# Kernel optimization log

Hardware: AMD Instinct MI355X
Metric: run time of the kernel (lower is better)

The kernel has to match this reference:

```python
import jax, jax.numpy as jnp
import numpy as np

EPS = 1e-5  # torch LayerNorm default eps

def _mish(x):
    return x * jnp.tanh(jax.nn.softplus(x))

def _ln(x, g, b):
    mu = jnp.mean(x, axis=-1, keepdims=True)
    var = jnp.mean(jnp.square(x - mu), axis=-1, keepdims=True)
    return (x - mu) * jax.lax.rsqrt(var + EPS) * g + b

def setup_inputs() -> dict:
    key = jax.random.key(0)
    ks = jax.random.split(key, 10)
    B, D, O1, O2, O3 = 65536, 784, 512, 264, 128
    def lin(k, fan_in, shape):
        bound = 1.0 / np.sqrt(fan_in)
        return jax.random.uniform(k, shape, jnp.float32, -bound, bound)
    return {
        "x":  jax.random.uniform(ks[0], (B, D), jnp.float32),
        "W1": lin(ks[1], D,  (O1, D)),   # enFC1, bias=False
        "g1": jnp.ones((O1,), jnp.float32), "b1": jnp.zeros((O1,), jnp.float32),
        "W2": lin(ks[2], O1, (O2, O1)),  # enFC2, bias=False
        "g2": jnp.ones((O2,), jnp.float32), "b2": jnp.zeros((O2,), jnp.float32),
        "W3": lin(ks[3], O2, (O3, O2)),  # enFC3 with bias
        "b3": lin(ks[4], O2, (O3,)),
        "gh": jnp.ones((O3,), jnp.float32), "bh": jnp.zeros((O3,), jnp.float32),
        "D1": lin(ks[5], O3, (O2, O3)),  # deFC1, bias=False
        "g3": jnp.ones((O2,), jnp.float32), "b3n": jnp.zeros((O2,), jnp.float32),
        "D2": lin(ks[6], O2, (O1, O2)),  # deFC2, bias=False
        "g4": jnp.ones((O1,), jnp.float32), "b4": jnp.zeros((O1,), jnp.float32),
        "D3": lin(ks[7], O1, (D, O1)),   # deFC3 with bias
        "bo": lin(ks[8], O1, (D,)),
    }

def reference(x, W1, g1, b1, W2, g2, b2, W3, b3, gh, bh,
              D1, g3, b3n, D2, g4, b4, D3, bo):
    h = _mish(_ln(x @ W1.T, g1, b1))
    h = _mish(_ln(h @ W2.T, g2, b2))
    x_latent = _mish(_ln(h @ W3.T + b3, gh, bh))
    h = _mish(_ln(x_latent @ D1.T, g3, b3n))
    h = _mish(_ln(h @ D2.T, g4, b4))
    out = jax.nn.sigmoid(h @ D3.T + bo)
    return out, jnp.sum(jnp.abs(x_latent))
```

## Files before the change

kernel.cpp:

```cpp
#include <hip/hip_runtime.h>


typedef short bf16x8 __attribute__((ext_vector_type(8)));
typedef float f32x4  __attribute__((ext_vector_type(4)));

#define B_ROWS 65536
#define EPS_LN 1e-5f

static __device__ __forceinline__ unsigned short f2bf(float f) {
    union { float f; unsigned u; } v; v.f = f;
    unsigned r = v.u + 0x7FFFu + ((v.u >> 16) & 1u);
    return (unsigned short)(r >> 16);
}

static __device__ __forceinline__ float mish_f(float x) {
    if (x > 15.f) return x;
    float u = __expf(x);
    float p = __fmaf_rn(u, u, 2.f * u);
    return x * (p / (p + 2.f));
}

static __device__ __forceinline__ void glds16(const void* g, void* l) {
    typedef __attribute__((address_space(3))) unsigned lds_u32;
    typedef __attribute__((address_space(1))) const unsigned glb_u32;
    lds_u32* lp = (lds_u32*)l;
    unsigned lofs = __builtin_amdgcn_readfirstlane((unsigned)(unsigned long long)lp);
    lp = (lds_u32*)(unsigned long long)lofs;
    __builtin_amdgcn_global_load_lds((glb_u32*)g, lp, 16, 0, 0);
}

struct CvtArgs {
    const float* src[6];
    unsigned short* dst[6];
    int O[6], K[6], KP[6];
    int base[7];
};

__global__ void wpad_kernel(CvtArgs a) {
    int b = blockIdx.x;
    int seg = 0;
    while (b >= a.base[seg + 1]) ++seg;
    int r = b - a.base[seg];
    int O = a.O[seg], K = a.K[seg], KP = a.KP[seg];
    const float* s = a.src[seg];
    unsigned short* d = a.dst[seg];
    for (int c = threadIdx.x; c < KP; c += 256) {
        unsigned short v = 0;
        if (r < O && c < K) v = f2bf(s[(size_t)r * K + c]);
        d[(size_t)r * KP + c] = v;
    }
}

template<int KP, int ASTR, int BN, int OREAL, int OSTRIDE, int NKT,
         bool SRCF32, bool HASBIAS, bool ABS, bool LN>
__global__ __launch_bounds__(512, 2)
void layer9(const void* __restrict__ Asrc,
            const unsigned short* __restrict__ Wp,
            const float* __restrict__ gam,
            const float* __restrict__ bet,
            const float* __restrict__ bias,
            void* __restrict__ Aout,
            float* __restrict__ partials)
{
    constexpr int NT   = BN / 64;
    constexpr int NCHW = BN / 8;
    constexpr int NCH  = NCHW + (SRCF32 ? 0 : 16);
    constexpr int MAXC = (NCH + 7) / 8;
    constexpr int ABY  = 128 * 128;
    constexpr int WBY  = BN * 128;

    __shared__ __align__(16) char smem[2 * ABY + 2 * WBY];

    const int tid  = threadIdx.x;
    const int lane = tid & 63;
    const int wu   = __builtin_amdgcn_readfirstlane(tid >> 6);
    const int wr = wu >> 2, wc = wu & 3;
    const int lg = lane >> 4, lc = lane & 15;
    const int row0  = blockIdx.x * 128;
    const int cbase = LN ? 0 : blockIdx.y * BN;

    const int crow = lane >> 3;
    const int sg   = (lane & 7) ^ crow;
    const size_t vofW = ((size_t)crow * KP + (size_t)(sg << 3)) * 2;
    const size_t vofA = ((size_t)crow * ASTR + (size_t)(sg << 3)) * 2;

    auto stage = [&](int t, int b) {
#pragma unroll
        for (int i = 0; i < MAXC; ++i) {
            int c = wu + 8 * i;
            if (c < NCHW) {
                const char* g = (const char*)Wp +
                    ((size_t)(cbase + c * 8) * KP) * 2 + (size_t)t * 128 + vofW;
                glds16(g, smem + (2 * ABY + b * WBY + c * 1024));
            } else if (c < NCH) {
                int ca = c - NCHW;
                const char* g = (const char*)Asrc +
                    ((size_t)(row0 + ca * 8) * ASTR) * 2 + (size_t)t * 128 + vofA;
                glds16(g, smem + (b * ABY + ca * 1024));
            }
        }
    };

    const int ar = tid >> 2, as = tid & 3;
    const float* axp = (const float*)Asrc + (size_t)(row0 + ar) * ASTR + as * 16;
    float4 rA[4];
#pragma unroll
    for (int j = 0; j < 4; ++j) rA[j] = make_float4(0, 0, 0, 0);

    auto loadA1 = [&](int t) {
#pragma unroll
        for (int j = 0; j < 4; ++j) {
            int c0 = t * 64 + as * 16 + j * 4;
            rA[j] = (c0 + 3 < 784) ? *(const float4*)(axp + t * 64 + j * 4)
                                   : make_float4(0, 0, 0, 0);
        }
    };
    auto pubA = [&](int b) {
        union { unsigned short us[8]; uint4 v; } u0, u1;
        u0.us[0] = f2bf(rA[0].x); u0.us[1] = f2bf(rA[0].y);
        u0.us[2] = f2bf(rA[0].z); u0.us[3] = f2bf(rA[0].w);
        u0.us[4] = f2bf(rA[1].x); u0.us[5] = f2bf(rA[1].y);
        u0.us[6] = f2bf(rA[1].z); u0.us[7] = f2bf(rA[1].w);
        u1.us[0] = f2bf(rA[2].x); u1.us[1] = f2bf(rA[2].y);
        u1.us[2] = f2bf(rA[2].z); u1.us[3] = f2bf(rA[2].w);
        u1.us[4] = f2bf(rA[3].x); u1.us[5] = f2bf(rA[3].y);
        u1.us[6] = f2bf(rA[3].z); u1.us[7] = f2bf(rA[3].w);
        int s0 = as * 2, rb = b * ABY + ar * 128, rx = ar & 7;
        *(uint4*)(smem + rb + (((s0    ) ^ rx) << 4)) = u0.v;
        *(uint4*)(smem + rb + (((s0 + 1) ^ rx) << 4)) = u1.v;
    };

    stage(0, 0);
    if constexpr (SRCF32) { loadA1(0); pubA(0); }
    __syncthreads();

    f32x4 acc[4][NT];
#pragma unroll
    for (int a = 0; a < 4; ++a)
#pragma unroll
        for (int c = 0; c < NT; ++c) acc[a][c] = (f32x4){0.f, 0.f, 0.f, 0.f};

    const int f0 = ((lg ^ (lc & 7)) << 4);

    for (int t = 0; t < NKT; ++t) {
        const int bsel = t & 1;
        if (t + 1 < NKT) {
            stage(t + 1, bsel ^ 1);
            if constexpr (SRCF32) loadA1(t + 1);
        }
        const char* Ab = smem + bsel * ABY + (wr * 64 + lc) * 128;
        const char* Bb = smem + 2 * ABY + bsel * WBY + (wc * NT * 16 + lc) * 128;
#pragma unroll
        for (int h = 0; h < 2; ++h) {
            const int fh = f0 ^ (h << 6);
            bf16x8 afr[4], bfr[NT];
#pragma unroll
            for (int a = 0; a < 4; ++a)
                afr[a] = *(const bf16x8*)(Ab + a * 2048 + fh);
#pragma unroll
            for (int c = 0; c < NT; ++c)
                bfr[c] = *(const bf16x8*)(Bb + c * 2048 + fh);
            __builtin_amdgcn_s_setprio(1);
#pragma unroll
            for (int c = 0; c < NT; ++c)
#pragma unroll
                for (int a = 0; a < 4; ++a)
                    acc[a][c] = __builtin_amdgcn_mfma_f32_16x16x32_bf16(afr[a], bfr[c], acc[a][c], 0, 0, 0);
            __builtin_amdgcn_s_setprio(0);
        }
        if constexpr (SRCF32) { if (t + 1 < NKT) pubA(bsel ^ 1); }
        __syncthreads();
    }

    if constexpr (LN) {
        if constexpr (HASBIAS) {
#pragma unroll
            for (int c = 0; c < NT; ++c) {
                int col = wc * NT * 16 + c * 16 + lc;
                float bv = (col < OREAL) ? bias[col] : 0.f;
#pragma unroll
                for (int a = 0; a < 4; ++a)
#pragma unroll
                    for (int r = 0; r < 4; ++r) acc[a][c][r] += bv;
            }
        }
        float ps1[4][4], ps2[4][4];
#pragma unroll
        for (int a = 0; a < 4; ++a)
#pragma unroll
            for (int r = 0; r < 4; ++r) { ps1[a][r] = 0.f; ps2[a][r] = 0.f; }
#pragma unroll
        for (int a = 0; a < 4; ++a)
#pragma unroll
            for (int c = 0; c < NT; ++c)
#pragma unroll
                for (int r = 0; r < 4; ++r) {
                    float v = acc[a][c][r];
                    ps1[a][r] += v;
                    ps2[a][r] = __fmaf_rn(v, v, ps2[a][r]);
                }
#pragma unroll
        for (int m = 1; m < 16; m <<= 1)
#pragma unroll
            for (int a = 0; a < 4; ++a)
#pragma unroll
                for (int r = 0; r < 4; ++r) {
                    ps1[a][r] += __shfl_xor(ps1[a][r], m);
                    ps2[a][r] += __shfl_xor(ps2[a][r], m);
                }

        float* lnP  = (float*)smem;
        float* lnMR = (float*)(smem + 4096);
        float* wsum = (float*)(smem + 5120);

        if (lc == 0) {
#pragma unroll
            for (int a = 0; a < 4; ++a)
#pragma unroll
                for (int r = 0; r < 4; ++r) {
                    int row = wr * 64 + a * 16 + lg * 4 + r;
                    lnP[row * 4 + wc]       = ps1[a][r];
                    lnP[512 + row * 4 + wc] = ps2[a][r];
                }
        }
        __syncthreads();
        if (tid < 128) {
            float s1 = lnP[tid * 4] + lnP[tid * 4 + 1] + lnP[tid * 4 + 2] + lnP[tid * 4 + 3];
            float s2 = lnP[512 + tid * 4] + lnP[512 + tid * 4 + 1] +
                       lnP[512 + tid * 4 + 2] + lnP[512 + tid * 4 + 3];
            float mu = s1 * (1.f / OREAL);
            float var = fmaxf(s2 * (1.f / OREAL) - mu * mu, 0.f);
            lnMR[tid]       = mu;
            lnMR[128 + tid] = rsqrtf(var + EPS_LN);
        }
        __syncthreads();

        float gcol[NT], bcol[NT];
#pragma unroll
        for (int c = 0; c < NT; ++c) {
            int col = wc * NT * 16 + c * 16 + lc;
            gcol[c] = (col < OREAL) ? gam[col] : 0.f;
            bcol[c] = (col < OREAL) ? bet[col] : 0.f;
        }

        float asum = 0.f;
        unsigned short* outp = (unsigned short*)Aout;
#pragma unroll
        for (int a = 0; a < 4; ++a)
#pragma unroll
            for (int r = 0; r < 4; ++r) {
                int rl = wr * 64 + a * 16 + lg * 4 + r;
                float mu = lnMR[rl], rs = lnMR[128 + rl];
                size_t rowoff = (size_t)(row0 + rl) * OSTRIDE;
#pragma unroll
                for (int c = 0; c < NT; ++c) {
                    int col = wc * NT * 16 + c * 16 + lc;
                    if (col < OSTRIDE) {
                        unsigned short outv = 0;
                        if (col < OREAL) {
                            float v = (acc[a][c][r] - mu) * rs * gcol[c] + bcol[c];
                            float mz = mish_f(v);
                            if (ABS) asum += fabsf(mz);
                            outv = f2bf(mz);
                        }
                        outp[rowoff + col] = outv;
                    }
                }
            }

        if constexpr (ABS) {
#pragma unroll
            for (int m = 1; m < 64; m <<= 1) asum += __shfl_xor(asum, m);
            if (lane == 0) wsum[wu] = asum;
            __syncthreads();
            if (tid == 0) {
                float s = 0.f;
                for (int w = 0; w < 8; ++w) s += wsum[w];
                partials[blockIdx.x] = s;
            }
        }
    } else {
        float* outp = (float*)Aout;
#pragma unroll
        for (int c = 0; c < NT; ++c) {
            int col = cbase + wc * NT * 16 + c * 16 + lc;
            bool ok = col < OREAL;
            float bv = ok ? bias[col] : 0.f;
#pragma unroll
            for (int a = 0; a < 4; ++a)
#pragma unroll
                for (int r = 0; r < 4; ++r) {
                    if (ok) {
                        int rl = wr * 64 + a * 16 + lg * 4 + r;
                        float v = acc[a][c][r] + bv;
                        outp[(size_t)(row0 + rl) * OSTRIDE + col] = 1.f / (1.f + __expf(-v));
                    }
                }
        }
    }
}

__global__ void reduce_abs(const float* __restrict__ partials, float* __restrict__ out) {
    __shared__ float sm[256];
    float s = 0.f;
    for (int i = threadIdx.x; i < 512; i += 256) s += partials[i];
    sm[threadIdx.x] = s;
    __syncthreads();
    for (int step = 128; step > 0; step >>= 1) {
        if (threadIdx.x < step) sm[threadIdx.x] += sm[threadIdx.x + step];
        __syncthreads();
    }
    if (threadIdx.x == 0) out[0] = sm[0];
}

extern "C" void kernel_launch(void* const* d_in, const int* in_sizes, int n_in,
                              void* d_out, int out_size, void* d_ws, size_t ws_size,
                              hipStream_t stream)
{
    const float* x   = (const float*)d_in[0];
    const float* W1  = (const float*)d_in[1];
    const float* g1  = (const float*)d_in[2];
    const float* b1  = (const float*)d_in[3];
    const float* W2  = (const float*)d_in[4];
    const float* g2  = (const float*)d_in[5];
    const float* b2  = (const float*)d_in[6];
    const float* W3  = (const float*)d_in[7];
    const float* b3  = (const float*)d_in[8];
    const float* gh  = (const float*)d_in[9];
    const float* bh  = (const float*)d_in[10];
    const float* D1  = (const float*)d_in[11];
    const float* g3  = (const float*)d_in[12];
    const float* b3n = (const float*)d_in[13];
    const float* D2  = (const float*)d_in[14];
    const float* g4  = (const float*)d_in[15];
    const float* b4  = (const float*)d_in[16];
    const float* D3  = (const float*)d_in[17];
    const float* bo  = (const float*)d_in[18];

    char* ws = (char*)d_ws;
    size_t off = 0;
    auto alloc = [&](size_t bytes) -> char* {
        char* p = ws + off;
        off += (bytes + 255) & ~(size_t)255;
        return p;
    };
    unsigned short* W1p = (unsigned short*)alloc((size_t)512 * 832 * 2);
    unsigned short* W2p = (unsigned short*)alloc((size_t)384 * 512 * 2);
    unsigned short* W3p = (unsigned short*)alloc((size_t)128 * 320 * 2);
    unsigned short* D1p = (unsigned short*)alloc((size_t)384 * 128 * 2);
    unsigned short* D2p = (unsigned short*)alloc((size_t)512 * 320 * 2);
    unsigned short* D3p = (unsigned short*)alloc((size_t)896 * 512 * 2);
    unsigned short* actP = (unsigned short*)alloc((size_t)B_ROWS * 512 * 2);
    unsigned short* actQ = (unsigned short*)alloc((size_t)B_ROWS * 320 * 2);
    unsigned short* actL = (unsigned short*)alloc((size_t)B_ROWS * 128 * 2);
    float* partials = (float*)alloc(512 * 4);

    CvtArgs ca;
    ca.src[0] = W1; ca.dst[0] = W1p; ca.O[0] = 512; ca.K[0] = 784; ca.KP[0] = 832;
    ca.src[1] = W2; ca.dst[1] = W2p; ca.O[1] = 264; ca.K[1] = 512; ca.KP[1] = 512;
    ca.src[2] = W3; ca.dst[2] = W3p; ca.O[2] = 128; ca.K[2] = 264; ca.KP[2] = 320;
    ca.src[3] = D1; ca.dst[3] = D1p; ca.O[3] = 264; ca.K[3] = 128; ca.KP[3] = 128;
    ca.src[4] = D2; ca.dst[4] = D2p; ca.O[4] = 512; ca.K[4] = 264; ca.KP[4] = 320;
    ca.src[5] = D3; ca.dst[5] = D3p; ca.O[5] = 784; ca.K[5] = 512; ca.KP[5] = 512;
    ca.base[0] = 0;    ca.base[1] = 512;  ca.base[2] = 896;
    ca.base[3] = 1024; ca.base[4] = 1408; ca.base[5] = 1920; ca.base[6] = 2816;
    wpad_kernel<<<2816, 256, 0, stream>>>(ca);

    const int NB = B_ROWS / 128;

    layer9<832, 784, 512, 512, 512, 13, true,  false, false, true>
        <<<NB, 512, 0, stream>>>(x, W1p, g1, b1, nullptr, actP, nullptr);
    layer9<512, 512, 384, 264, 320, 8,  false, false, false, true>
        <<<NB, 512, 0, stream>>>(actP, W2p, g2, b2, nullptr, actQ, nullptr);
    layer9<320, 320, 128, 128, 128, 5,  false, true,  true,  true>
        <<<NB, 512, 0, stream>>>(actQ, W3p, gh, bh, b3, actL, partials);
    layer9<128, 128, 384, 264, 320, 2,  false, false, false, true>
        <<<NB, 512, 0, stream>>>(actL, D1p, g3, b3n, nullptr, actQ, nullptr);
    layer9<320, 320, 512, 512, 512, 5,  false, false, false, true>
        <<<NB, 512, 0, stream>>>(actQ, D2p, g4, b4, nullptr, actP, nullptr);
    dim3 g6(NB, 2);
    layer9<512, 512, 448, 784, 784, 8,  false, true,  false, false>
        <<<g6, 512, 0, stream>>>(actP, D3p, nullptr, nullptr, bo, d_out, nullptr);

    reduce_abs<<<1, 256, 0, stream>>>(partials, (float*)d_out + (size_t)B_ROWS * 784);
}
```

Measured before the change: 426.9 us.

## Split K-loop into four barriered phases interleaving staging with MFMA

Restructures the GEMM main loop of every layer into four sub-phases (two K-halves times two column halves). Global-to-LDS staging is split into two groups issued between phases, with explicit s_barrier and lgkmcnt/vmcnt waits replacing the single __syncthreads. The fp32 input load for the first layer is prefetched two tiles ahead. The aim is to overlap memory traffic with matrix-core work and keep the waves in step, at the cost of more barriers and tighter hand-written wait counts, which could break correctness or stall if the counts are wrong.

```diff
diff --git a/kernel.cpp b/kernel.cpp
--- a/kernel.cpp
+++ b/kernel.cpp
@@ -28,6 +28,16 @@
     lp = (lds_u32*)(unsigned long long)lofs;
     __builtin_amdgcn_global_load_lds((glb_u32*)g, lp, 16, 0, 0);
 }
+
+template<int N> __device__ __forceinline__ void vwait() {
+    if constexpr      (N <= 0) asm volatile("s_waitcnt vmcnt(0)" ::: "memory");
+    else if constexpr (N == 4) asm volatile("s_waitcnt vmcnt(4)" ::: "memory");
+    else                       asm volatile("s_waitcnt vmcnt(8)" ::: "memory");
+}
+
+#define LGKM0 do { asm volatile("s_waitcnt lgkmcnt(0)" ::: "memory"); \
+                   __builtin_amdgcn_sched_barrier(0); } while (0)
+#define PBAR  __builtin_amdgcn_s_barrier()
 
 struct CvtArgs {
     const float* src[6];
@@ -54,18 +64,19 @@
 template<int KP, int ASTR, int BN, int OREAL, int OSTRIDE, int NKT,
          bool SRCF32, bool HASBIAS, bool ABS, bool LN>
 __global__ __launch_bounds__(512, 2)
-void layer9(const void* __restrict__ Asrc,
-            const unsigned short* __restrict__ Wp,
-            const float* __restrict__ gam,
-            const float* __restrict__ bet,
-            const float* __restrict__ bias,
-            void* __restrict__ Aout,
-            float* __restrict__ partials)
+void layer10(const void* __restrict__ Asrc,
+             const unsigned short* __restrict__ Wp,
+             const float* __restrict__ gam,
+             const float* __restrict__ bet,
+             const float* __restrict__ bias,
+             void* __restrict__ Aout,
+             float* __restrict__ partials)
 {
     constexpr int NT   = BN / 64;
+    constexpr int CH0  = (NT + 1) / 2;
+    constexpr int CH1  = NT - CH0;
     constexpr int NCHW = BN / 8;
-    constexpr int NCH  = NCHW + (SRCF32 ? 0 : 16);
-    constexpr int MAXC = (NCH + 7) / 8;
+    constexpr int NWCH = NCHW / 8;
     constexpr int ABY  = 128 * 128;
     constexpr int WBY  = BN * 128;
 
@@ -84,20 +95,21 @@
     const size_t vofW = ((size_t)crow * KP + (size_t)(sg << 3)) * 2;
     const size_t vofA = ((size_t)crow * ASTR + (size_t)(sg << 3)) * 2;
 
-    auto stage = [&](int t, int b) {
-#pragma unroll
-        for (int i = 0; i < MAXC; ++i) {
-            int c = wu + 8 * i;
-            if (c < NCHW) {
-                const char* g = (const char*)Wp +
+    auto stage_grp = [&](int t, int b, int g) {
+#pragma unroll
+        for (int i = 0; i < NWCH; ++i) {
+            if ((i & 1) == g) {
+                int c = wu + 8 * i;
+                const char* gp = (const char*)Wp +
                     ((size_t)(cbase + c * 8) * KP) * 2 + (size_t)t * 128 + vofW;
-                glds16(g, smem + (2 * ABY + b * WBY + c * 1024));
-            } else if (c < NCH) {
-                int ca = c - NCHW;
-                const char* g = (const char*)Asrc +
-                    ((size_t)(row0 + ca * 8) * ASTR) * 2 + (size_t)t * 128 + vofA;
-                glds16(g, smem + (b * ABY + ca * 1024));
+                glds16(gp, smem + (2 * ABY + b * WBY + c * 1024));
             }
+        }
+        if constexpr (!SRCF32) {
+            int ca = wu + 8 * g;
+            const char* gp = (const char*)Asrc +
+                ((size_t)(row0 + ca * 8) * ASTR) * 2 + (size_t)t * 128 + vofA;
+            glds16(gp, smem + (b * ABY + ca * 1024));
         }
     };
 
@@ -130,8 +142,12 @@
         *(uint4*)(smem + rb + (((s0 + 1) ^ rx) << 4)) = u1.v;
     };
 
-    stage(0, 0);
-    if constexpr (SRCF32) { loadA1(0); pubA(0); }
+    stage_grp(0, 0, 0);
+    stage_grp(0, 0, 1);
+    if constexpr (SRCF32) {
+        loadA1(0); pubA(0);
+        if (NKT > 1) loadA1(1);
+    }
     __syncthreads();
 
     f32x4 acc[4][NT];
@@ -143,33 +159,71 @@
     const int f0 = ((lg ^ (lc & 7)) << 4);
 
     for (int t = 0; t < NKT; ++t) {
-        const int bsel = t & 1;
-        if (t + 1 < NKT) {
-            stage(t + 1, bsel ^ 1);
-            if constexpr (SRCF32) loadA1(t + 1);
-        }
+        const int bsel = t & 1, nb = bsel ^ 1;
+        const bool pre = (t + 1 < NKT);
         const char* Ab = smem + bsel * ABY + (wr * 64 + lc) * 128;
         const char* Bb = smem + 2 * ABY + bsel * WBY + (wc * NT * 16 + lc) * 128;
-#pragma unroll
-        for (int h = 0; h < 2; ++h) {
-            const int fh = f0 ^ (h << 6);
-            bf16x8 afr[4], bfr[NT];
-#pragma unroll
-            for (int a = 0; a < 4; ++a)
-                afr[a] = *(const bf16x8*)(Ab + a * 2048 + fh);
-#pragma unroll
-            for (int c = 0; c < NT; ++c)
-                bfr[c] = *(const bf16x8*)(Bb + c * 2048 + fh);
-            __builtin_amdgcn_s_setprio(1);
-#pragma unroll
-            for (int c = 0; c < NT; ++c)
-#pragma unroll
-                for (int a = 0; a < 4; ++a)
-                    acc[a][c] = __builtin_amdgcn_mfma_f32_16x16x32_bf16(afr[a], bfr[c], acc[a][c], 0, 0, 0);
-            __builtin_amdgcn_s_setprio(0);
-        }
-        if constexpr (SRCF32) { if (t + 1 < NKT) pubA(bsel ^ 1); }
-        __syncthreads();
+
+        bf16x8 afr[4], bfr0[CH0], bfr1[CH1 > 0 ? CH1 : 1];
+
+#pragma unroll
+        for (int a = 0; a < 4; ++a) afr[a] = *(const bf16x8*)(Ab + a * 2048 + f0);
+#pragma unroll
+        for (int c = 0; c < CH0; ++c) bfr0[c] = *(const bf16x8*)(Bb + c * 2048 + f0);
+        if (pre) stage_grp(t + 1, nb, 0);
+        PBAR; LGKM0;
+        __builtin_amdgcn_s_setprio(1);
+#pragma unroll
+        for (int c = 0; c < CH0; ++c)
+#pragma unroll
+            for (int a = 0; a < 4; ++a)
+                acc[a][c] = __builtin_amdgcn_mfma_f32_16x16x32_bf16(afr[a], bfr0[c], acc[a][c], 0, 0, 0);
+        __builtin_amdgcn_s_setprio(0);
+        PBAR;
+
+#pragma unroll
+        for (int c = 0; c < CH1; ++c) bfr1[c] = *(const bf16x8*)(Bb + (CH0 + c) * 2048 + f0);
+        if (pre) stage_grp(t + 1, nb, 1);
+        PBAR; LGKM0;
+        __builtin_amdgcn_s_setprio(1);
+#pragma unroll
+        for (int c = 0; c < CH1; ++c)
+#pragma unroll
+            for (int a = 0; a < 4; ++a)
+                acc[a][CH0 + c] = __builtin_amdgcn_mfma_f32_16x16x32_bf16(afr[a], bfr1[c], acc[a][CH0 + c], 0, 0, 0);
+        __builtin_amdgcn_s_setprio(0);
+        PBAR;
+
+#pragma unroll
+        for (int a = 0; a < 4; ++a) afr[a] = *(const bf16x8*)(Ab + a * 2048 + (f0 ^ 64));
+#pragma unroll
+        for (int c = 0; c < CH0; ++c) bfr0[c] = *(const bf16x8*)(Bb + c * 2048 + (f0 ^ 64));
+        PBAR; LGKM0;
+        __builtin_amdgcn_s_setprio(1);
+#pragma unroll
+        for (int c = 0; c < CH0; ++c)
+#pragma unroll
+            for (int a = 0; a < 4; ++a)
+                acc[a][c] = __builtin_amdgcn_mfma_f32_16x16x32_bf16(afr[a], bfr0[c], acc[a][c], 0, 0, 0);
+        __builtin_amdgcn_s_setprio(0);
+        PBAR;
+
+#pragma unroll
+        for (int c = 0; c < CH1; ++c) bfr1[c] = *(const bf16x8*)(Bb + (CH0 + c) * 2048 + (f0 ^ 64));
+        if constexpr (SRCF32) {
+            if (pre) pubA(nb);
+            if (t + 2 < NKT) loadA1(t + 2);
+        }
+        PBAR; LGKM0;
+        __builtin_amdgcn_s_setprio(1);
+#pragma unroll
+        for (int c = 0; c < CH1; ++c)
+#pragma unroll
+            for (int a = 0; a < 4; ++a)
+                acc[a][CH0 + c] = __builtin_amdgcn_mfma_f32_16x16x32_bf16(afr[a], bfr1[c], acc[a][CH0 + c], 0, 0, 0);
+        __builtin_amdgcn_s_setprio(0);
+        vwait<SRCF32 ? 4 : 0>();
+        PBAR;
     }
 
     if constexpr (LN) {
@@ -368,18 +422,18 @@
 
     const int NB = B_ROWS / 128;
 
-    layer9<832, 784, 512, 512, 512, 13, true,  false, false, true>
+    layer10<832, 784, 512, 512, 512, 13, true,  false, false, true>
         <<<NB, 512, 0, stream>>>(x, W1p, g1, b1, nullptr, actP, nullptr);
-    layer9<512, 512, 384, 264, 320, 8,  false, false, false, true>
+    layer10<512, 512, 384, 264, 320, 8,  false, false, false, true>
         <<<NB, 512, 0, stream>>>(actP, W2p, g2, b2, nullptr, actQ, nullptr);
-    layer9<320, 320, 128, 128, 128, 5,  false, true,  true,  true>
+    layer10<320, 320, 128, 128, 128, 5,  false, true,  true,  true>
         <<<NB, 512, 0, stream>>>(actQ, W3p, gh, bh, b3, actL, partials);
-    layer9<128, 128, 384, 264, 320, 2,  false, false, false, true>
+    layer10<128, 128, 384, 264, 320, 2,  false, false, false, true>
         <<<NB, 512, 0, stream>>>(actL, D1p, g3, b3n, nullptr, actQ, nullptr);
-    layer9<320, 320, 512, 512, 512, 5,  false, false, false, true>
+    layer10<320, 320, 512, 512, 512, 5,  false, false, false, true>
         <<<NB, 512, 0, stream>>>(actQ, D2p, g4, b4, nullptr, actP, nullptr);
     dim3 g6(NB, 2);
-    layer9<512, 512, 448, 784, 784, 8,  false, true,  false, false>
+    layer10<512, 512, 448, 784, 784, 8,  false, true,  false, false>
         <<<g6, 512, 0, stream>>>(actP, D3p, nullptr, nullptr, bo, d_out, nullptr);
 
     reduce_abs<<<1, 256, 0, stream>>>(partials, (float*)d_out + (size_t)B_ROWS * 784);
```

New measurement: 431.8 us. About the same (+1.1%).

## Switch GEMM tiles to 32x32x16 MFMA and split final layer launch

Applied to the files above, without the earlier changes.

Each wave now computes its output tile with 32x32x16 bf16 MFMA blocks (2 row blocks × BN/128 column blocks) instead of 16x16x32 blocks. The LDS fragment loads, swizzle offsets, LayerNorm row reductions and epilogue row and column mapping are all rewritten for the 32x32 accumulator layout. The larger MFMA shape cuts LDS fragment reads and instruction count per flop, and the wider shuffle reduction covers 32 lanes. The last decoder layer also changes from one 2-D grid with 448-column halves to two launches of 512 and 384 columns with an explicit column base, which adds a kernel launch.

```diff
diff --git a/kernel.cpp b/kernel.cpp
--- a/kernel.cpp
+++ b/kernel.cpp
@@ -1,8 +1,8 @@
 #include <hip/hip_runtime.h>
 
 
-typedef short bf16x8 __attribute__((ext_vector_type(8)));
-typedef float f32x4  __attribute__((ext_vector_type(4)));
+typedef short bf16x8  __attribute__((ext_vector_type(8)));
+typedef float f32x16  __attribute__((ext_vector_type(16)));
 
 #define B_ROWS 65536
 #define EPS_LN 1e-5f
@@ -54,15 +54,16 @@
 template<int KP, int ASTR, int BN, int OREAL, int OSTRIDE, int NKT,
          bool SRCF32, bool HASBIAS, bool ABS, bool LN>
 __global__ __launch_bounds__(512, 2)
-void layer9(const void* __restrict__ Asrc,
-            const unsigned short* __restrict__ Wp,
-            const float* __restrict__ gam,
-            const float* __restrict__ bet,
-            const float* __restrict__ bias,
-            void* __restrict__ Aout,
-            float* __restrict__ partials)
+void layer11(const void* __restrict__ Asrc,
+             const unsigned short* __restrict__ Wp,
+             const float* __restrict__ gam,
+             const float* __restrict__ bet,
+             const float* __restrict__ bias,
+             void* __restrict__ Aout,
+             float* __restrict__ partials,
+             int cbase)
 {
-    constexpr int NT   = BN / 64;
+    constexpr int CI   = BN / 128;
     constexpr int NCHW = BN / 8;
     constexpr int NCH  = NCHW + (SRCF32 ? 0 : 16);
     constexpr int MAXC = (NCH + 7) / 8;
@@ -75,9 +76,8 @@
     const int lane = tid & 63;
     const int wu   = __builtin_amdgcn_readfirstlane(tid >> 6);
     const int wr = wu >> 2, wc = wu & 3;
-    const int lg = lane >> 4, lc = lane & 15;
-    const int row0  = blockIdx.x * 128;
-    const int cbase = LN ? 0 : blockIdx.y * BN;
+    const int l31 = lane & 31, h = lane >> 5;
+    const int row0 = blockIdx.x * 128;
 
     const int crow = lane >> 3;
     const int sg   = (lane & 7) ^ crow;
@@ -134,13 +134,17 @@
     if constexpr (SRCF32) { loadA1(0); pubA(0); }
     __syncthreads();
 
-    f32x4 acc[4][NT];
-#pragma unroll
-    for (int a = 0; a < 4; ++a)
-#pragma unroll
-        for (int c = 0; c < NT; ++c) acc[a][c] = (f32x4){0.f, 0.f, 0.f, 0.f};
-
-    const int f0 = ((lg ^ (lc & 7)) << 4);
+    f32x16 acc[2][CI];
+#pragma unroll
+    for (int ri = 0; ri < 2; ++ri)
+#pragma unroll
+        for (int ci = 0; ci < CI; ++ci)
+#pragma unroll
+            for (int e = 0; e < 16; ++e) acc[ri][ci][e] = 0.f;
+
+    int swz[4];
+#pragma unroll
+    for (int ks = 0; ks < 4; ++ks) swz[ks] = (((ks * 2 + h) ^ (l31 & 7)) << 4);
 
     for (int t = 0; t < NKT; ++t) {
         const int bsel = t & 1;
@@ -148,24 +152,24 @@
             stage(t + 1, bsel ^ 1);
             if constexpr (SRCF32) loadA1(t + 1);
         }
-        const char* Ab = smem + bsel * ABY + (wr * 64 + lc) * 128;
-        const char* Bb = smem + 2 * ABY + bsel * WBY + (wc * NT * 16 + lc) * 128;
-#pragma unroll
-        for (int h = 0; h < 2; ++h) {
-            const int fh = f0 ^ (h << 6);
-            bf16x8 afr[4], bfr[NT];
-#pragma unroll
-            for (int a = 0; a < 4; ++a)
-                afr[a] = *(const bf16x8*)(Ab + a * 2048 + fh);
-#pragma unroll
-            for (int c = 0; c < NT; ++c)
-                bfr[c] = *(const bf16x8*)(Bb + c * 2048 + fh);
+        const char* Ab = smem + bsel * ABY + (wr * 64 + l31) * 128;
+        const char* Bb = smem + 2 * ABY + bsel * WBY + (wc * CI * 32 + l31) * 128;
+#pragma unroll
+        for (int ks = 0; ks < 4; ++ks) {
+            bf16x8 afr[2], bfr[CI];
+#pragma unroll
+            for (int ri = 0; ri < 2; ++ri)
+                afr[ri] = *(const bf16x8*)(Ab + ri * 4096 + swz[ks]);
+#pragma unroll
+            for (int ci = 0; ci < CI; ++ci)
+                bfr[ci] = *(const bf16x8*)(Bb + ci * 4096 + swz[ks]);
             __builtin_amdgcn_s_setprio(1);
 #pragma unroll
-            for (int c = 0; c < NT; ++c)
-#pragma unroll
-                for (int a = 0; a < 4; ++a)
-                    acc[a][c] = __builtin_amdgcn_mfma_f32_16x16x32_bf16(afr[a], bfr[c], acc[a][c], 0, 0, 0);
+            for (int ci = 0; ci < CI; ++ci)
+#pragma unroll
+                for (int ri = 0; ri < 2; ++ri)
+                    acc[ri][ci] = __builtin_amdgcn_mfma_f32_32x32x16_bf16(
+                        afr[ri], bfr[ci], acc[ri][ci], 0, 0, 0);
             __builtin_amdgcn_s_setprio(0);
         }
         if constexpr (SRCF32) { if (t + 1 < NKT) pubA(bsel ^ 1); }
@@ -175,53 +179,48 @@
     if constexpr (LN) {
         if constexpr (HASBIAS) {
 #pragma unroll
-            for (int c = 0; c < NT; ++c) {
-                int col = wc * NT * 16 + c * 16 + lc;
+            for (int ci = 0; ci < CI; ++ci) {
+                int col = wc * CI * 32 + ci * 32 + l31;
                 float bv = (col < OREAL) ? bias[col] : 0.f;
 #pragma unroll
-                for (int a = 0; a < 4; ++a)
-#pragma unroll
-                    for (int r = 0; r < 4; ++r) acc[a][c][r] += bv;
-            }
-        }
-        float ps1[4][4], ps2[4][4];
-#pragma unroll
-        for (int a = 0; a < 4; ++a)
-#pragma unroll
-            for (int r = 0; r < 4; ++r) { ps1[a][r] = 0.f; ps2[a][r] = 0.f; }
-#pragma unroll
-        for (int a = 0; a < 4; ++a)
-#pragma unroll
-            for (int c = 0; c < NT; ++c)
-#pragma unroll
-                for (int r = 0; r < 4; ++r) {
-                    float v = acc[a][c][r];
-                    ps1[a][r] += v;
-                    ps2[a][r] = __fmaf_rn(v, v, ps2[a][r]);
-                }
-#pragma unroll
-        for (int m = 1; m < 16; m <<= 1)
-#pragma unroll
-            for (int a = 0; a < 4; ++a)
-#pragma unroll
-                for (int r = 0; r < 4; ++r) {
-                    ps1[a][r] += __shfl_xor(ps1[a][r], m);
-                    ps2[a][r] += __shfl_xor(ps2[a][r], m);
-                }
+                for (int ri = 0; ri < 2; ++ri)
+#pragma unroll
+                    for (int r = 0; r < 16; ++r) acc[ri][ci][r] += bv;
+            }
+        }
 
         float* lnP  = (float*)smem;
         float* lnMR = (float*)(smem + 4096);
         float* wsum = (float*)(smem + 5120);
 
-        if (lc == 0) {
-#pragma unroll
-            for (int a = 0; a < 4; ++a)
-#pragma unroll
-                for (int r = 0; r < 4; ++r) {
-                    int row = wr * 64 + a * 16 + lg * 4 + r;
-                    lnP[row * 4 + wc]       = ps1[a][r];
-                    lnP[512 + row * 4 + wc] = ps2[a][r];
-                }
+#pragma unroll
+        for (int ri = 0; ri < 2; ++ri) {
+            float s1[16], s2[16];
+#pragma unroll
+            for (int r = 0; r < 16; ++r) { s1[r] = 0.f; s2[r] = 0.f; }
+#pragma unroll
+            for (int ci = 0; ci < CI; ++ci)
+#pragma unroll
+                for (int r = 0; r < 16; ++r) {
+                    float v = acc[ri][ci][r];
+                    s1[r] += v;
+                    s2[r] = __fmaf_rn(v, v, s2[r]);
+                }
+#pragma unroll
+            for (int m = 1; m < 32; m <<= 1)
+#pragma unroll
+                for (int r = 0; r < 16; ++r) {
+                    s1[r] += __shfl_xor(s1[r], m);
+                    s2[r] += __shfl_xor(s2[r], m);
+                }
+            if (l31 == 0) {
+#pragma unroll
+                for (int r = 0; r < 16; ++r) {
+                    int row = wr * 64 + ri * 32 + (r & 3) + 8 * (r >> 2) + 4 * h;
+                    lnP[row * 4 + wc]       = s1[r];
+                    lnP[512 + row * 4 + wc] = s2[r];
+                }
+            }
         }
         __syncthreads();
         if (tid < 128) {
@@ -235,30 +234,30 @@
         }
         __syncthreads();
 
-        float gcol[NT], bcol[NT];
-#pragma unroll
-        for (int c = 0; c < NT; ++c) {
-            int col = wc * NT * 16 + c * 16 + lc;
-            gcol[c] = (col < OREAL) ? gam[col] : 0.f;
-            bcol[c] = (col < OREAL) ? bet[col] : 0.f;
+        float gcol[CI], bcol[CI];
+#pragma unroll
+        for (int ci = 0; ci < CI; ++ci) {
+            int col = wc * CI * 32 + ci * 32 + l31;
+            gcol[ci] = (col < OREAL) ? gam[col] : 0.f;
+            bcol[ci] = (col < OREAL) ? bet[col] : 0.f;
         }
 
         float asum = 0.f;
         unsigned short* outp = (unsigned short*)Aout;
 #pragma unroll
-        for (int a = 0; a < 4; ++a)
-#pragma unroll
-            for (int r = 0; r < 4; ++r) {
-                int rl = wr * 64 + a * 16 + lg * 4 + r;
+        for (int ri = 0; ri < 2; ++ri)
+#pragma unroll
+            for (int r = 0; r < 16; ++r) {
+                int rl = wr * 64 + ri * 32 + (r & 3) + 8 * (r >> 2) + 4 * h;
                 float mu = lnMR[rl], rs = lnMR[128 + rl];
                 size_t rowoff = (size_t)(row0 + rl) * OSTRIDE;
 #pragma unroll
-                for (int c = 0; c < NT; ++c) {
-                    int col = wc * NT * 16 + c * 16 + lc;
+                for (int ci = 0; ci < CI; ++ci) {
+                    int col = wc * CI * 32 + ci * 32 + l31;
                     if (col < OSTRIDE) {
                         unsigned short outv = 0;
                         if (col < OREAL) {
-                            float v = (acc[a][c][r] - mu) * rs * gcol[c] + bcol[c];
+                            float v = (acc[ri][ci][r] - mu) * rs * gcol[ci] + bcol[ci];
                             float mz = mish_f(v);
                             if (ABS) asum += fabsf(mz);
                             outv = f2bf(mz);
@@ -282,17 +281,17 @@
     } else {
         float* outp = (float*)Aout;
 #pragma unroll
-        for (int c = 0; c < NT; ++c) {
-            int col = cbase + wc * NT * 16 + c * 16 + lc;
+        for (int ci = 0; ci < CI; ++ci) {
+            int col = cbase + wc * CI * 32 + ci * 32 + l31;
             bool ok = col < OREAL;
             float bv = ok ? bias[col] : 0.f;
 #pragma unroll
-            for (int a = 0; a < 4; ++a)
-#pragma unroll
-                for (int r = 0; r < 4; ++r) {
+            for (int ri = 0; ri < 2; ++ri)
+#pragma unroll
+                for (int r = 0; r < 16; ++r) {
                     if (ok) {
-                        int rl = wr * 64 + a * 16 + lg * 4 + r;
-                        float v = acc[a][c][r] + bv;
+                        int rl = wr * 64 + ri * 32 + (r & 3) + 8 * (r >> 2) + 4 * h;
+                        float v = acc[ri][ci][r] + bv;
                         outp[(size_t)(row0 + rl) * OSTRIDE + col] = 1.f / (1.f + __expf(-v));
                     }
                 }
@@ -368,19 +367,20 @@
 
     const int NB = B_ROWS / 128;
 
-    layer9<832, 784, 512, 512, 512, 13, true,  false, false, true>
-        <<<NB, 512, 0, stream>>>(x, W1p, g1, b1, nullptr, actP, nullptr);
-    layer9<512, 512, 384, 264, 320, 8,  false, false, false, true>
-        <<<NB, 512, 0, stream>>>(actP, W2p, g2, b2, nullptr, actQ, nullptr);
-    layer9<320, 320, 128, 128, 128, 5,  false, true,  true,  true>
-        <<<NB, 512, 0, stream>>>(actQ, W3p, gh, bh, b3, actL, partials);
-    layer9<128, 128, 384, 264, 320, 2,  false, false, false, true>
-        <<<NB, 512, 0, stream>>>(actL, D1p, g3, b3n, nullptr, actQ, nullptr);
-    layer9<320, 320, 512, 512, 512, 5,  false, false, false, true>
-        <<<NB, 512, 0, stream>>>(actQ, D2p, g4, b4, nullptr, actP, nullptr);
-    dim3 g6(NB, 2);
-    layer9<512, 512, 448, 784, 784, 8,  false, true,  false, false>
-        <<<g6, 512, 0, stream>>>(actP, D3p, nullptr, nullptr, bo, d_out, nullptr);
+    layer11<832, 784, 512, 512, 512, 13, true,  false, false, true>
+        <<<NB, 512, 0, stream>>>(x, W1p, g1, b1, nullptr, actP, nullptr, 0);
+    layer11<512, 512, 384, 264, 320, 8,  false, false, false, true>
+        <<<NB, 512, 0, stream>>>(actP, W2p, g2, b2, nullptr, actQ, nullptr, 0);
+    layer11<320, 320, 128, 128, 128, 5,  false, true,  true,  true>
+        <<<NB, 512, 0, stream>>>(actQ, W3p, gh, bh, b3, actL, partials, 0);
+    layer11<128, 128, 384, 264, 320, 2,  false, false, false, true>
+        <<<NB, 512, 0, stream>>>(actL, D1p, g3, b3n, nullptr, actQ, nullptr, 0);
+    layer11<320, 320, 512, 512, 512, 5,  false, false, false, true>
+        <<<NB, 512, 0, stream>>>(actQ, D2p, g4, b4, nullptr, actP, nullptr, 0);
+    layer11<512, 512, 512, 784, 784, 8,  false, true,  false, false>
+        <<<NB, 512, 0, stream>>>(actP, D3p, nullptr, nullptr, bo, d_out, nullptr, 0);
+    layer11<512, 512, 384, 784, 784, 8,  false, true,  false, false>
+        <<<NB, 512, 0, stream>>>(actP, D3p, nullptr, nullptr, bo, d_out, nullptr, 512);
 
     reduce_abs<<<1, 256, 0, stream>>>(partials, (float*)d_out + (size_t)B_ROWS * 784);
 }
```

Result: slower. 489.3 us (+14.6%).

## Halve K tile to 32 and shrink K padding of weights and activations

Applied to the files above, without the earlier changes.

Each pipeline stage of the fused GEMM+LayerNorm+Mish layers now covers a 32-wide K slice instead of 64, halving the LDS footprint per buffer and adjusting the swizzle pattern for 64-byte rows. This lets the padded K dimensions shrink (832→800, 320→288), cutting wasted MFMA work and activation traffic on the padded 264-wide layers. In exchange there are twice as many loop iterations and __syncthreads barriers per tile, with less work available to hide each barrier.

```diff
diff --git a/kernel.cpp b/kernel.cpp
--- a/kernel.cpp
+++ b/kernel.cpp
@@ -54,20 +54,20 @@
 template<int KP, int ASTR, int BN, int OREAL, int OSTRIDE, int NKT,
          bool SRCF32, bool HASBIAS, bool ABS, bool LN>
 __global__ __launch_bounds__(512, 2)
-void layer9(const void* __restrict__ Asrc,
-            const unsigned short* __restrict__ Wp,
-            const float* __restrict__ gam,
-            const float* __restrict__ bet,
-            const float* __restrict__ bias,
-            void* __restrict__ Aout,
-            float* __restrict__ partials)
+void layer12(const void* __restrict__ Asrc,
+             const unsigned short* __restrict__ Wp,
+             const float* __restrict__ gam,
+             const float* __restrict__ bet,
+             const float* __restrict__ bias,
+             void* __restrict__ Aout,
+             float* __restrict__ partials)
 {
     constexpr int NT   = BN / 64;
-    constexpr int NCHW = BN / 8;
-    constexpr int NCH  = NCHW + (SRCF32 ? 0 : 16);
+    constexpr int NCHW = BN / 16;
+    constexpr int NCH  = NCHW + (SRCF32 ? 0 : 8);
     constexpr int MAXC = (NCH + 7) / 8;
-    constexpr int ABY  = 128 * 128;
-    constexpr int WBY  = BN * 128;
+    constexpr int ABY  = 128 * 64;
+    constexpr int WBY  = BN * 64;
 
     __shared__ __align__(16) char smem[2 * ABY + 2 * WBY];
 
@@ -79,10 +79,9 @@
     const int row0  = blockIdx.x * 128;
     const int cbase = LN ? 0 : blockIdx.y * BN;
 
-    const int crow = lane >> 3;
-    const int sg   = (lane & 7) ^ crow;
-    const size_t vofW = ((size_t)crow * KP + (size_t)(sg << 3)) * 2;
-    const size_t vofA = ((size_t)crow * ASTR + (size_t)(sg << 3)) * 2;
+    const int sg = (lane & 3) ^ ((lane >> 3) & 3);
+    const size_t vofW = ((size_t)(lane >> 2) * KP + (size_t)(sg << 3)) * 2;
+    const size_t vofA = ((size_t)(lane >> 2) * ASTR + (size_t)(sg << 3)) * 2;
 
     auto stage = [&](int t, int b) {
 #pragma unroll
@@ -90,44 +89,34 @@
             int c = wu + 8 * i;
             if (c < NCHW) {
                 const char* g = (const char*)Wp +
-                    ((size_t)(cbase + c * 8) * KP) * 2 + (size_t)t * 128 + vofW;
+                    ((size_t)(cbase + c * 16) * KP) * 2 + (size_t)t * 64 + vofW;
                 glds16(g, smem + (2 * ABY + b * WBY + c * 1024));
             } else if (c < NCH) {
                 int ca = c - NCHW;
                 const char* g = (const char*)Asrc +
-                    ((size_t)(row0 + ca * 8) * ASTR) * 2 + (size_t)t * 128 + vofA;
+                    ((size_t)(row0 + ca * 16) * ASTR) * 2 + (size_t)t * 64 + vofA;
                 glds16(g, smem + (b * ABY + ca * 1024));
             }
         }
     };
 
     const int ar = tid >> 2, as = tid & 3;
-    const float* axp = (const float*)Asrc + (size_t)(row0 + ar) * ASTR + as * 16;
-    float4 rA[4];
-#pragma unroll
-    for (int j = 0; j < 4; ++j) rA[j] = make_float4(0, 0, 0, 0);
+    const float* axp = (const float*)Asrc + (size_t)(row0 + ar) * ASTR + as * 8;
+    const int aswz = ar * 64 + ((as ^ ((ar >> 1) & 3)) << 4);
+    float4 rA0 = make_float4(0, 0, 0, 0), rA1 = make_float4(0, 0, 0, 0);
 
     auto loadA1 = [&](int t) {
-#pragma unroll
-        for (int j = 0; j < 4; ++j) {
-            int c0 = t * 64 + as * 16 + j * 4;
-            rA[j] = (c0 + 3 < 784) ? *(const float4*)(axp + t * 64 + j * 4)
-                                   : make_float4(0, 0, 0, 0);
-        }
+        int c0 = t * 32 + as * 8;
+        rA0 = (c0     < 784) ? *(const float4*)(axp + t * 32)     : make_float4(0, 0, 0, 0);
+        rA1 = (c0 + 4 < 784) ? *(const float4*)(axp + t * 32 + 4) : make_float4(0, 0, 0, 0);
     };
     auto pubA = [&](int b) {
-        union { unsigned short us[8]; uint4 v; } u0, u1;
-        u0.us[0] = f2bf(rA[0].x); u0.us[1] = f2bf(rA[0].y);
-        u0.us[2] = f2bf(rA[0].z); u0.us[3] = f2bf(rA[0].w);
-        u0.us[4] = f2bf(rA[1].x); u0.us[5] = f2bf(rA[1].y);
-        u0.us[6] = f2bf(rA[1].z); u0.us[7] = f2bf(rA[1].w);
-        u1.us[0] = f2bf(rA[2].x); u1.us[1] = f2bf(rA[2].y);
-        u1.us[2] = f2bf(rA[2].z); u1.us[3] = f2bf(rA[2].w);
-        u1.us[4] = f2bf(rA[3].x); u1.us[5] = f2bf(rA[3].y);
-        u1.us[6] = f2bf(rA[3].z); u1.us[7] = f2bf(rA[3].w);
-        int s0 = as * 2, rb = b * ABY + ar * 128, rx = ar & 7;
-        *(uint4*)(smem + rb + (((s0    ) ^ rx) << 4)) = u0.v;
-        *(uint4*)(smem + rb + (((s0 + 1) ^ rx) << 4)) = u1.v;
+        union { unsigned short us[8]; uint4 v; } u;
+        u.us[0] = f2bf(rA0.x); u.us[1] = f2bf(rA0.y);
+        u.us[2] = f2bf(rA0.z); u.us[3] = f2bf(rA0.w);
+        u.us[4] = f2bf(rA1.x); u.us[5] = f2bf(rA1.y);
+        u.us[6] = f2bf(rA1.z); u.us[7] = f2bf(rA1.w);
+        *(uint4*)(smem + b * ABY + aswz) = u.v;
     };
 
     stage(0, 0);
@@ -140,7 +129,7 @@
 #pragma unroll
         for (int c = 0; c < NT; ++c) acc[a][c] = (f32x4){0.f, 0.f, 0.f, 0.f};
 
-    const int f0 = ((lg ^ (lc & 7)) << 4);
+    const int fswz = ((lg ^ ((lc >> 1) & 3)) << 4);
 
     for (int t = 0; t < NKT; ++t) {
         const int bsel = t & 1;
@@ -148,26 +137,20 @@
             stage(t + 1, bsel ^ 1);
             if constexpr (SRCF32) loadA1(t + 1);
         }
-        const char* Ab = smem + bsel * ABY + (wr * 64 + lc) * 128;
-        const char* Bb = smem + 2 * ABY + bsel * WBY + (wc * NT * 16 + lc) * 128;
-#pragma unroll
-        for (int h = 0; h < 2; ++h) {
-            const int fh = f0 ^ (h << 6);
-            bf16x8 afr[4], bfr[NT];
+        const char* Ab = smem + bsel * ABY + (wr * 64 + lc) * 64 + fswz;
+        const char* Bb = smem + 2 * ABY + bsel * WBY + (wc * NT * 16 + lc) * 64 + fswz;
+        bf16x8 afr[4], bfr[NT];
+#pragma unroll
+        for (int a = 0; a < 4; ++a) afr[a] = *(const bf16x8*)(Ab + a * 1024);
+#pragma unroll
+        for (int c = 0; c < NT; ++c) bfr[c] = *(const bf16x8*)(Bb + c * 1024);
+        __builtin_amdgcn_s_setprio(1);
+#pragma unroll
+        for (int c = 0; c < NT; ++c)
 #pragma unroll
             for (int a = 0; a < 4; ++a)
-                afr[a] = *(const bf16x8*)(Ab + a * 2048 + fh);
-#pragma unroll
-            for (int c = 0; c < NT; ++c)
-                bfr[c] = *(const bf16x8*)(Bb + c * 2048 + fh);
-            __builtin_amdgcn_s_setprio(1);
-#pragma unroll
-            for (int c = 0; c < NT; ++c)
-#pragma unroll
-                for (int a = 0; a < 4; ++a)
-                    acc[a][c] = __builtin_amdgcn_mfma_f32_16x16x32_bf16(afr[a], bfr[c], acc[a][c], 0, 0, 0);
-            __builtin_amdgcn_s_setprio(0);
-        }
+                acc[a][c] = __builtin_amdgcn_mfma_f32_16x16x32_bf16(afr[a], bfr[c], acc[a][c], 0, 0, 0);
+        __builtin_amdgcn_s_setprio(0);
         if constexpr (SRCF32) { if (t + 1 < NKT) pubA(bsel ^ 1); }
         __syncthreads();
     }
@@ -344,23 +327,23 @@
         off += (bytes + 255) & ~(size_t)255;
         return p;
     };
-    unsigned short* W1p = (unsigned short*)alloc((size_t)512 * 832 * 2);
+    unsigned short* W1p = (unsigned short*)alloc((size_t)512 * 800 * 2);
     unsigned short* W2p = (unsigned short*)alloc((size_t)384 * 512 * 2);
-    unsigned short* W3p = (unsigned short*)alloc((size_t)128 * 320 * 2);
+    unsigned short* W3p = (unsigned short*)alloc((size_t)128 * 288 * 2);
     unsigned short* D1p = (unsigned short*)alloc((size_t)384 * 128 * 2);
-    unsigned short* D2p = (unsigned short*)alloc((size_t)512 * 320 * 2);
+    unsigned short* D2p = (unsigned short*)alloc((size_t)512 * 288 * 2);
     unsigned short* D3p = (unsigned short*)alloc((size_t)896 * 512 * 2);
     unsigned short* actP = (unsigned short*)alloc((size_t)B_ROWS * 512 * 2);
-    unsigned short* actQ = (unsigned short*)alloc((size_t)B_ROWS * 320 * 2);
+    unsigned short* actQ = (unsigned short*)alloc((size_t)B_ROWS * 288 * 2);
     unsigned short* actL = (unsigned short*)alloc((size_t)B_ROWS * 128 * 2);
     float* partials = (float*)alloc(512 * 4);
 
     CvtArgs ca;
-    ca.src[0] = W1; ca.dst[0] = W1p; ca.O[0] = 512; ca.K[0] = 784; ca.KP[0] = 832;
+    ca.src[0] = W1; ca.dst[0] = W1p; ca.O[0] = 512; ca.K[0] = 784; ca.KP[0] = 800;
     ca.src[1] = W2; ca.dst[1] = W2p; ca.O[1] = 264; ca.K[1] = 512; ca.KP[1] = 512;
-    ca.src[2] = W3; ca.dst[2] = W3p; ca.O[2] = 128; ca.K[2] = 264; ca.KP[2] = 320;
+    ca.src[2] = W3; ca.dst[2] = W3p; ca.O[2] = 128; ca.K[2] = 264; ca.KP[2] = 288;
     ca.src[3] = D1; ca.dst[3] = D1p; ca.O[3] = 264; ca.K[3] = 128; ca.KP[3] = 128;
-    ca.src[4] = D2; ca.dst[4] = D2p; ca.O[4] = 512; ca.K[4] = 264; ca.KP[4] = 320;
+    ca.src[4] = D2; ca.dst[4] = D2p; ca.O[4] = 512; ca.K[4] = 264; ca.KP[4] = 288;
     ca.src[5] = D3; ca.dst[5] = D3p; ca.O[5] = 784; ca.K[5] = 512; ca.KP[5] = 512;
     ca.base[0] = 0;    ca.base[1] = 512;  ca.base[2] = 896;
     ca.base[3] = 1024; ca.base[4] = 1408; ca.base[5] = 1920; ca.base[6] = 2816;
@@ -368,18 +351,18 @@
 
     const int NB = B_ROWS / 128;
 
-    layer9<832, 784, 512, 512, 512, 13, true,  false, false, true>
+    layer12<800, 784, 512, 512, 512, 25, true,  false, false, true>
         <<<NB, 512, 0, stream>>>(x, W1p, g1, b1, nullptr, actP, nullptr);
-    layer9<512, 512, 384, 264, 320, 8,  false, false, false, true>
+    layer12<512, 512, 384, 264, 288, 16, false, false, false, true>
         <<<NB, 512, 0, stream>>>(actP, W2p, g2, b2, nullptr, actQ, nullptr);
-    layer9<320, 320, 128, 128, 128, 5,  false, true,  true,  true>
+    layer12<288, 288, 128, 128, 128, 9,  false, true,  true,  true>
         <<<NB, 512, 0, stream>>>(actQ, W3p, gh, bh, b3, actL, partials);
-    layer9<128, 128, 384, 264, 320, 2,  false, false, false, true>
+    layer12<128, 128, 384, 264, 288, 4,  false, false, false, true>
         <<<NB, 512, 0, stream>>>(actL, D1p, g3, b3n, nullptr, actQ, nullptr);
-    layer9<320, 320, 512, 512, 512, 5,  false, false, false, true>
+    layer12<288, 288, 512, 512, 512, 9,  false, false, false, true>
         <<<NB, 512, 0, stream>>>(actQ, D2p, g4, b4, nullptr, actP, nullptr);
     dim3 g6(NB, 2);
-    layer9<512, 512, 448, 784, 784, 8,  false, true,  false, false>
+    layer12<512, 512, 448, 784, 784, 16, false, true,  false, false>
         <<<g6, 512, 0, stream>>>(actP, D3p, nullptr, nullptr, bo, d_out, nullptr);
 
     reduce_abs<<<1, 256, 0, stream>>>(partials, (float*)d_out + (size_t)B_ROWS * 784);
```

Result: slower. 488.2 us (+14.4%).
